# Optimization experiments

Hardware: AMD Instinct MI355X
Metric: run time of the kernel (lower is better)

The kernel has to match this reference:

```python
import jax, jax.numpy as jnp
import numpy as np

N_NODES = 50000
N_EDGES = 800000
IN_CH, HID_CH, OUT_CH = 128, 256, 128


def setup_inputs() -> dict:
    key = jax.random.key(0)
    ks = jax.random.split(key, 9)
    x = jax.random.normal(ks[0], (N_NODES, IN_CH), dtype=jnp.float32)
    edge_index = jax.random.randint(ks[1], (2, N_EDGES), 0, N_NODES, dtype=jnp.int64)
    # SAGEConv params: lin_l (aggregated neighbors, with bias), lin_r (root, no bias)
    s1 = 1.0 / np.sqrt(IN_CH)
    s2 = 1.0 / np.sqrt(HID_CH)
    W1_l = jax.random.uniform(ks[2], (IN_CH, HID_CH), jnp.float32, -s1, s1)
    W1_r = jax.random.uniform(ks[3], (IN_CH, HID_CH), jnp.float32, -s1, s1)
    b1 = jax.random.uniform(ks[4], (HID_CH,), jnp.float32, -s1, s1)
    W2_l = jax.random.uniform(ks[5], (HID_CH, OUT_CH), jnp.float32, -s2, s2)
    W2_r = jax.random.uniform(ks[6], (HID_CH, OUT_CH), jnp.float32, -s2, s2)
    b2 = jax.random.uniform(ks[7], (OUT_CH,), jnp.float32, -s2, s2)
    return {"x": x, "edge_index": edge_index, "W1_l": W1_l, "W1_r": W1_r,
            "b1": b1, "W2_l": W2_l, "W2_r": W2_r, "b2": b2}


def _sage_conv(x, edge_index, Wl, Wr, b):
    # PyG SAGEConv: out = lin_l(mean_{j in N(i)} x_j) + lin_r(x_i)
    src, dst = edge_index[0], edge_index[1]
    msg = x[src]                                                    # [E, C] gather
    agg = jax.ops.segment_sum(msg, dst, num_segments=x.shape[0])    # [N, C] scatter-add
    cnt = jax.ops.segment_sum(jnp.ones((src.shape[0],), x.dtype), dst,
                              num_segments=x.shape[0])              # [N]
    agg = agg / jnp.maximum(cnt, 1.0)[:, None]                      # mean; deg-0 -> 0
    return agg @ Wl + x @ Wr + b


def reference(x, edge_index, W1_l, W1_r, b1, W2_l, W2_r, b2):
    h = jax.nn.relu(_sage_conv(x, edge_index, W1_l, W1_r, b1))
    # dropout(p=0.5) is stochastic; use eval-mode identity for a deterministic baseline
    out = _sage_conv(h, edge_index, W2_l, W2_r, b2)
    return jax.nn.log_softmax(out, axis=1)
```

## Files before the change

### kernel.cpp

```cpp
#include <hip/hip_runtime.h>
#include <math.h>

#define NN 50000
#define NE 800000
#define BINW 256
#define NB ((NN + BINW - 1) / BINW)
#define CAP 4864
#define CHUNK 4096
#define NBIN ((NE + CHUNK - 1) / CHUNK)
#define NXB 6250
#define NWB 256
#define EPT 16

typedef __attribute__((ext_vector_type(8))) _Float16 f16x8;
typedef __attribute__((ext_vector_type(2))) _Float16 h2;
typedef __attribute__((ext_vector_type(4))) float f32x4;
typedef unsigned int uint32;
typedef __attribute__((address_space(3))) unsigned int lds_uint;
typedef const __attribute__((address_space(1))) unsigned int glb_uint;

__device__ inline unsigned short f2h(float f) {
    _Float16 h = (_Float16)f;
    return __builtin_bit_cast(unsigned short, h);
}
__device__ inline uint32 pack2h(float a, float b) {
    return (uint32)f2h(a) | ((uint32)f2h(b) << 16);
}
__device__ inline h2 as_h2(uint32 u) { return __builtin_bit_cast(h2, u); }

__device__ inline int edge_at(const void* edges, int is64, int i) {
    return is64 ? (int)((const long long*)edges)[i] : ((const int*)edges)[i];
}

__global__ void k_zero(int* bcnt) {
    int i = threadIdx.x;
    if (i < NB) bcnt[i] = 0;
}

__global__ __launch_bounds__(256)
void k_front(const void* __restrict__ edges, uint32* __restrict__ gbuf,
             int* __restrict__ bcnt,
             const float* __restrict__ x, unsigned short* __restrict__ A1,
             const float* __restrict__ W1l, const float* __restrict__ W1r,
             const float* __restrict__ W2l, const float* __restrict__ W2r,
             unsigned short* __restrict__ B1t, unsigned short* __restrict__ B2t) {
    int b = blockIdx.x;
    if (b >= NBIN) {
        if (b < NBIN + NXB) {
            int t = (b - NBIN) * 256 + threadIdx.x;
            if (t >= NN * 32) return;
            int node = t >> 5, q = t & 31;
            float4 v = *(const float4*)(x + (size_t)node * 128 + q * 4);
            *(uint2*)(A1 + (size_t)node * 256 + 128 + q * 4) =
                make_uint2(pack2h(v.x, v.y), pack2h(v.z, v.w));
        } else {
            int t = (b - NBIN - NXB) * 256 + threadIdx.x;
            int n = t >> 8, k = t & 255;
            float v1 = (k < 128) ? W1l[k * 256 + n] : W1r[(k - 128) * 256 + n];
            B1t[n * 256 + k] = f2h(v1);
            float v2 = (n < 128) ? W2l[k * 128 + n] : W2r[k * 128 + (n - 128)];
            B2t[n * 256 + k] = f2h(v2);
        }
        return;
    }
    __shared__ int hist[NB], excl[NB], cur[NB], gpos[NB];
    __shared__ int is64s;
    __shared__ uint32 sorted[CHUNK];
    int t = threadIdx.x;
    int base = b * CHUNK;
    int n = NE - base; if (n > CHUNK) n = CHUNK;
    if (t < 64) {
        const long long* q = (const long long*)edges;
        long long v = q[t];
        unsigned long long m = __ballot(v >= 0 && v < NN);
        if (t == 0) is64s = (m == ~0ull) ? 1 : 0;
    }
    for (int i = t; i < NB; i += 256) hist[i] = 0;
    __syncthreads();
    int is64 = is64s;
    int sA[EPT], dA[EPT];
    #pragma unroll
    for (int q = 0; q < EPT; ++q) {
        int i = t + q * 256;
        if (i < n) {
            sA[q] = edge_at(edges, is64, base + i);
            dA[q] = edge_at(edges, is64, NE + base + i);
        } else dA[q] = -1;
    }
    #pragma unroll
    for (int q = 0; q < EPT; ++q)
        if (dA[q] >= 0) atomicAdd(&hist[dA[q] >> 8], 1);
    __syncthreads();
    if (t == 0) {
        int s = 0;
        for (int k = 0; k < NB; ++k) { excl[k] = s; s += hist[k]; }
    }
    __syncthreads();
    for (int i = t; i < NB; i += 256) {
        gpos[i] = atomicAdd(&bcnt[i], hist[i]);
        cur[i] = excl[i];
    }
    __syncthreads();
    #pragma unroll
    for (int q = 0; q < EPT; ++q) {
        if (dA[q] >= 0) {
            int bk = dA[q] >> 8;
            int lp = atomicAdd(&cur[bk], 1);
            sorted[lp] = ((uint32)(dA[q] & (BINW - 1)) << 16) | (uint32)sA[q];
        }
    }
    __syncthreads();
    for (int i = t; i < n; i += 256) {
        int lo = 0, hi = NB - 1;
        while (lo < hi) { int mid = (lo + hi + 1) >> 1; if (excl[mid] <= i) lo = mid; else hi = mid - 1; }
        int gp = gpos[lo] + (i - excl[lo]);
        if (gp < CAP) gbuf[(size_t)lo * CAP + gp] = sorted[i];
    }
}

__global__ __launch_bounds__(256) void k_sort(const uint32* __restrict__ gbuf,
                                              const int* __restrict__ bcnt,
                                              int* __restrict__ offs,
                                              unsigned short* __restrict__ ssrc) {
    __shared__ int hist[BINW], cur[BINW], wsum[4];
    __shared__ int sorted[CAP];
    __shared__ int bb_s;
    int b = blockIdx.x, t = threadIdx.x;
    int lane = t & 63, w = t >> 6;
    int c = (t < NB) ? bcnt[t] : 0;
    int pre = (t < b) ? c : 0;
    #pragma unroll
    for (int s = 1; s < 64; s <<= 1) pre += __shfl_xor(pre, s);
    if (lane == 0) wsum[w] = pre;
    hist[t] = 0;
    __syncthreads();
    if (t == 0) bb_s = wsum[0] + wsum[1] + wsum[2] + wsum[3];
    __syncthreads();
    int bb = bb_s;
    int cnt = bcnt[b]; if (cnt > CAP) cnt = CAP;
    int nbase = b * BINW;
    int ncnt = NN - nbase; if (ncnt > BINW) ncnt = BINW;
    for (int i = t; i < cnt; i += 256)
        atomicAdd(&hist[gbuf[(size_t)b * CAP + i] >> 16], 1);
    __syncthreads();
    int d = hist[t];
    int v = d;
    #pragma unroll
    for (int s = 1; s < 64; s <<= 1) { int x = __shfl_up(v, s); if (lane >= s) v += x; }
    if (lane == 63) wsum[w] = v;
    __syncthreads();
    if (t == 0) { int s = 0; for (int i = 0; i < 4; ++i) { int x = wsum[i]; wsum[i] = s; s += x; } }
    __syncthreads();
    int excl = wsum[w] + (v - d);
    if (t < ncnt) offs[nbase + t] = bb + excl;
    if (b == NB - 1 && t == 0) offs[NN] = NE;
    cur[t] = excl;
    __syncthreads();
    for (int i = t; i < cnt; i += 256) {
        uint32 p = gbuf[(size_t)b * CAP + i];
        int lp = atomicAdd(&cur[p >> 16], 1);
        sorted[lp] = (int)(p & 0xFFFFu);
    }
    __syncthreads();
    for (int i = t; i < cnt; i += 256)
        ssrc[bb + i] = (unsigned short)sorted[i];
}

#define ACCH(vv) { a[0] += as_h2((vv).x); a[1] += as_h2((vv).y); \
                   a[2] += as_h2((vv).z); a[3] += as_h2((vv).w); }

__device__ inline void burst_gather4(const unsigned short* __restrict__ tab, int coff,
                                     const unsigned short* __restrict__ ssrc, int s0, int s1,
                                     int lane, h2* a) {
    int grp = lane >> 4, cl = lane & 15;
    const unsigned short* bp = tab + coff + cl * 8;
    int e = s0;
    while (e < s1) {
        int cnt = s1 - e; if (cnt > 64) cnt = 64;
        int myidx = (lane < cnt) ? (int)ssrc[e + lane] : 0;
        for (int r0 = 0; r0 < cnt; r0 += 32) {
            uint4 v[8]; bool ok[8];
            #pragma unroll
            for (int u = 0; u < 8; ++u) {
                int r = r0 + u * 4 + grp;
                ok[u] = r < cnt;
                int s = __shfl(myidx, r & 63);
                v[u] = *(const uint4*)(bp + (size_t)s * 256);
            }
            #pragma unroll
            for (int u = 0; u < 8; ++u) if (ok[u]) ACCH(v[u]);
        }
        e += cnt;
    }
}

__device__ inline void xreduce_h(h2* a) {
    #pragma unroll
    for (int k = 0; k < 4; ++k) {
        uint32 u = __builtin_bit_cast(uint32, a[k]);
        a[k] += as_h2((uint32)__shfl_xor((int)u, 16));
        u = __builtin_bit_cast(uint32, a[k]);
        a[k] += as_h2((uint32)__shfl_xor((int)u, 32));
    }
}

__global__ void k_agg(unsigned short* __restrict__ A1, const int* __restrict__ offs,
                      const unsigned short* __restrict__ ssrc) {
    int node = blockIdx.x * 4 + (threadIdx.x >> 6);
    int lane = threadIdx.x & 63;
    if (node >= NN) return;
    int cl = lane & 15;
    int s0 = offs[node], s1 = offs[node + 1];
    h2 a[4] = {};
    burst_gather4(A1, 128, ssrc, s0, s1, lane, a);
    xreduce_h(a);
    float inv = 1.0f / fmaxf((float)(s1 - s0), 1.0f);
    if (lane < 16) {
        uint4 p;
        p.x = pack2h((float)a[0][0] * inv, (float)a[0][1] * inv);
        p.y = pack2h((float)a[1][0] * inv, (float)a[1][1] * inv);
        p.z = pack2h((float)a[2][0] * inv, (float)a[2][1] * inv);
        p.w = pack2h((float)a[3][0] * inv, (float)a[3][1] * inv);
        *(uint4*)(A1 + (size_t)node * 256 + cl * 8) = p;
    }
}

template <bool RELU>
__global__ __launch_bounds__(256)
void k_gemm_bf(const unsigned short* __restrict__ A, const unsigned short* __restrict__ Bt,
               const float* __restrict__ bias, unsigned short* __restrict__ C) {
    __shared__ unsigned short AsmL[3][128 * 32];
    __shared__ unsigned short BsmL[3][128 * 32];
    int t = threadIdx.x;
    int lane = t & 63, w = t >> 6;
    int m0 = blockIdx.x * 128, n0 = blockIdx.y * 128;
    int wr = (w >> 1) * 64, wc = (w & 1) * 64;
    int fr = lane & 15, fk = (lane >> 4) * 8;

    f32x4 acc[4][4] = {};
    int srow = lane >> 2;
    int scol = (lane & 3) * 8;
    auto STAGE = [&](int bufi, int ks) {
        #pragma unroll
        for (int q = 0; q < 2; ++q) {
            int widx = w * 2 + q;
            int row = widx * 16 + srow;
            const unsigned short* ga = A + (size_t)(m0 + row) * 256 + ks * 32 + scol;
            __builtin_amdgcn_global_load_lds((glb_uint*)ga, (lds_uint*)&AsmL[bufi][widx * 512], 16, 0, 0);
            const unsigned short* gb = Bt + (size_t)(n0 + row) * 256 + ks * 32 + scol;
            __builtin_amdgcn_global_load_lds((glb_uint*)gb, (lds_uint*)&BsmL[bufi][widx * 512], 16, 0, 0);
        }
    };

    STAGE(0, 0);
    STAGE(1, 1);
    #pragma unroll
    for (int ks = 0; ks < 8; ++ks) {
        if (ks < 7) asm volatile("s_waitcnt vmcnt(4)" ::: "memory");
        else        asm volatile("s_waitcnt vmcnt(0)" ::: "memory");
        __builtin_amdgcn_s_barrier();
        __builtin_amdgcn_sched_barrier(0);
        if (ks < 6) STAGE((ks + 2) % 3, ks + 2);
        int cb = ks % 3;
        f16x8 af[4], bfr[4];
        #pragma unroll
        for (int i = 0; i < 4; ++i) af[i] = *(const f16x8*)&AsmL[cb][(wr + i * 16 + fr) * 32 + fk];
        #pragma unroll
        for (int j = 0; j < 4; ++j) bfr[j] = *(const f16x8*)&BsmL[cb][(wc + j * 16 + fr) * 32 + fk];
        #pragma unroll
        for (int i = 0; i < 4; ++i)
            #pragma unroll
            for (int j = 0; j < 4; ++j)
                acc[i][j] = __builtin_amdgcn_mfma_f32_16x16x32_f16(af[i], bfr[j], acc[i][j], 0, 0, 0);
    }

    int r0 = (lane >> 4) * 4;
    #pragma unroll
    for (int i = 0; i < 4; ++i) {
        #pragma unroll
        for (int j = 0; j < 4; ++j) {
            int gn = n0 + wc + j * 16 + fr;
            float bb = RELU ? bias[gn] : 0.f;
            #pragma unroll
            for (int rr = 0; rr < 4; ++rr) {
                int gm = m0 + wr + i * 16 + r0 + rr;
                if (gm >= NN) continue;
                float v = acc[i][j][rr];
                if (RELU) v = fmaxf(v + bb, 0.f);
                C[(size_t)gm * 256 + gn] = f2h(v);
            }
        }
    }
}

__global__ void k_final(const unsigned short* __restrict__ P, const int* __restrict__ offs,
                        const unsigned short* __restrict__ ssrc, const float* __restrict__ b2,
                        float* __restrict__ out) {
    int node = blockIdx.x * 4 + (threadIdx.x >> 6);
    int lane = threadIdx.x & 63;
    if (node >= NN) return;
    int cl = lane & 15;
    int s0 = offs[node], s1 = offs[node + 1];
    h2 a[4] = {};
    burst_gather4(P, 0, ssrc, s0, s1, lane, a);
    xreduce_h(a);
    float inv = 1.0f / fmaxf((float)(s1 - s0), 1.0f);
    uint4 rv = *(const uint4*)(P + (size_t)node * 256 + 128 + cl * 8);
    float4 ba = *(const float4*)(b2 + cl * 8);
    float4 bb = *(const float4*)(b2 + cl * 8 + 4);
    h2 r0 = as_h2(rv.x), r1 = as_h2(rv.y), r2 = as_h2(rv.z), r3 = as_h2(rv.w);
    float vv[8];
    vv[0] = (float)a[0][0] * inv + (float)r0[0] + ba.x;
    vv[1] = (float)a[0][1] * inv + (float)r0[1] + ba.y;
    vv[2] = (float)a[1][0] * inv + (float)r1[0] + ba.z;
    vv[3] = (float)a[1][1] * inv + (float)r1[1] + ba.w;
    vv[4] = (float)a[2][0] * inv + (float)r2[0] + bb.x;
    vv[5] = (float)a[2][1] * inv + (float)r2[1] + bb.y;
    vv[6] = (float)a[3][0] * inv + (float)r3[0] + bb.z;
    vv[7] = (float)a[3][1] * inv + (float)r3[1] + bb.w;

    float mx = vv[0];
    #pragma unroll
    for (int k = 1; k < 8; ++k) mx = fmaxf(mx, vv[k]);
    #pragma unroll
    for (int d = 1; d < 16; d <<= 1) mx = fmaxf(mx, __shfl_xor(mx, d));
    float s = 0.f;
    #pragma unroll
    for (int k = 0; k < 8; ++k) s += __expf(vv[k] - mx);
    #pragma unroll
    for (int d = 1; d < 16; d <<= 1) s += __shfl_xor(s, d);
    float ls = logf(s);
    if (lane < 16) {
        float4 o0 = make_float4(vv[0] - mx - ls, vv[1] - mx - ls, vv[2] - mx - ls, vv[3] - mx - ls);
        float4 o1 = make_float4(vv[4] - mx - ls, vv[5] - mx - ls, vv[6] - mx - ls, vv[7] - mx - ls);
        *(float4*)(out + (size_t)node * 128 + cl * 8) = o0;
        *(float4*)(out + (size_t)node * 128 + cl * 8 + 4) = o1;
    }
}

extern "C" void kernel_launch(void* const* d_in, const int* in_sizes, int n_in,
                              void* d_out, int out_size, void* d_ws, size_t ws_size,
                              hipStream_t stream) {
    const float* x   = (const float*)d_in[0];
    const void*  edg = d_in[1];
    const float* W1l = (const float*)d_in[2];
    const float* W1r = (const float*)d_in[3];
    const float* b1  = (const float*)d_in[4];
    const float* W2l = (const float*)d_in[5];
    const float* W2r = (const float*)d_in[6];
    const float* b2  = (const float*)d_in[7];
    float* out = (float*)d_out;

    char* ws = (char*)d_ws;
    size_t off = 0;
    auto alloc = [&](size_t bytes) {
        size_t cur = off;
        off = (off + bytes + 255) & ~(size_t)255;
        return cur;
    };
    int* bcnt  = (int*)(ws + alloc((size_t)NB * 4));
    int* offs  = (int*)(ws + alloc((size_t)(NN + 1) * 4));
    unsigned short* ssrc = (unsigned short*)(ws + alloc((size_t)NE * 2));
    uint32* gbuf = (uint32*)(ws + alloc((size_t)NB * CAP * 4));
    unsigned short* A1  = (unsigned short*)(ws + alloc((size_t)NN * 256 * 2));
    unsigned short* Hb  = (unsigned short*)(ws + alloc((size_t)NN * 256 * 2));
    unsigned short* Pb  = (unsigned short*)(ws + alloc((size_t)NN * 256 * 2));
    unsigned short* B1t = (unsigned short*)(ws + alloc((size_t)65536 * 2));
    unsigned short* B2t = (unsigned short*)(ws + alloc((size_t)65536 * 2));
    (void)alloc(65536);

    int nb_w = (NN + 3) / 4;
    int mblocks = (NN + 127) / 128;

    k_zero<<<1, 256, 0, stream>>>(bcnt);
    k_front<<<NBIN + NXB + NWB, 256, 0, stream>>>(edg, gbuf, bcnt, x, A1,
                                                  W1l, W1r, W2l, W2r, B1t, B2t);
    k_sort<<<NB, 256, 0, stream>>>(gbuf, bcnt, offs, ssrc);
    k_agg<<<nb_w, 256, 0, stream>>>(A1, offs, ssrc);
    k_gemm_bf<true><<<dim3(mblocks, 2), 256, 0, stream>>>(A1, B1t, b1, Hb);
    k_gemm_bf<false><<<dim3(mblocks, 2), 256, 0, stream>>>(Hb, B2t, nullptr, Pb);
    k_final<<<nb_w, 256, 0, stream>>>(Pb, offs, ssrc, b2, out);
}
```

Measured before the change: 147.7 us.

## Map four nodes per wavefront in aggregation and final gather kernels

Each 64-lane wavefront now handles four nodes, with one 16-lane group per node, instead of one node per wavefront with a cross-group shuffle reduction. Neighbor indices are staged in registers and broadcast with shuffles, and degrees above 32 fall back to direct index loads. This removes the xor-shuffle reduction and the idle lanes during stores, and cuts the grid to a quarter of its size. In exchange, the loop runs to the maximum degree among the four nodes, which adds divergence, and the launch relies on NN being divisible by 16 with no bounds check.

```diff
diff --git a/kernel.cpp b/kernel.cpp
--- a/kernel.cpp
+++ b/kernel.cpp
@@ -166,63 +166,60 @@
         ssrc[bb + i] = (unsigned short)sorted[i];
 }
 
-#define ACCH(vv) { a[0] += as_h2((vv).x); a[1] += as_h2((vv).y); \
-                   a[2] += as_h2((vv).z); a[3] += as_h2((vv).w); }
-
-__device__ inline void burst_gather4(const unsigned short* __restrict__ tab, int coff,
-                                     const unsigned short* __restrict__ ssrc, int s0, int s1,
-                                     int lane, h2* a) {
-    int grp = lane >> 4, cl = lane & 15;
-    const unsigned short* bp = tab + coff + cl * 8;
-    int e = s0;
-    while (e < s1) {
-        int cnt = s1 - e; if (cnt > 64) cnt = 64;
-        int myidx = (lane < cnt) ? (int)ssrc[e + lane] : 0;
-        for (int r0 = 0; r0 < cnt; r0 += 32) {
-            uint4 v[8]; bool ok[8];
-            #pragma unroll
-            for (int u = 0; u < 8; ++u) {
-                int r = r0 + u * 4 + grp;
-                ok[u] = r < cnt;
-                int s = __shfl(myidx, r & 63);
-                v[u] = *(const uint4*)(bp + (size_t)s * 256);
-            }
-            #pragma unroll
-            for (int u = 0; u < 8; ++u) if (ok[u]) ACCH(v[u]);
-        }
-        e += cnt;
-    }
-}
-
-__device__ inline void xreduce_h(h2* a) {
-    #pragma unroll
-    for (int k = 0; k < 4; ++k) {
-        uint32 u = __builtin_bit_cast(uint32, a[k]);
-        a[k] += as_h2((uint32)__shfl_xor((int)u, 16));
-        u = __builtin_bit_cast(uint32, a[k]);
-        a[k] += as_h2((uint32)__shfl_xor((int)u, 32));
+#define ACCH1(vv) { a[0] += as_h2((vv).x); a[1] += as_h2((vv).y); \
+                    a[2] += as_h2((vv).z); a[3] += as_h2((vv).w); }
+
+__device__ inline void group_gather(const unsigned short* __restrict__ tab, int coff,
+                                    const unsigned short* __restrict__ ssrc,
+                                    int s0, int deg, int md, int grp, int lig, h2* a) {
+    const unsigned short* bp = tab + coff + lig * 8;
+    int idxA = (lig < deg)      ? (int)ssrc[s0 + lig]      : 0;
+    int idxB = (16 + lig < deg) ? (int)ssrc[s0 + 16 + lig] : 0;
+    int cap = md < 32 ? md : 32;
+    for (int i0 = 0; i0 < cap; i0 += 8) {
+        uint4 v[8];
+        #pragma unroll
+        for (int u = 0; u < 8; ++u) {
+            int i = i0 + u;
+            int word = (i & 16) ? idxB : idxA;
+            int s = __shfl(word, grp * 16 + (i & 15));
+            v[u] = *(const uint4*)(bp + (size_t)s * 256);
+        }
+        #pragma unroll
+        for (int u = 0; u < 8; ++u) if (i0 + u < deg) ACCH1(v[u]);
+    }
+    for (int i0 = 32; i0 < md; i0 += 4) {
+        uint4 v[4];
+        #pragma unroll
+        for (int u = 0; u < 4; ++u) {
+            int i = i0 + u;
+            int s = (i < deg) ? (int)ssrc[s0 + i] : 0;
+            v[u] = *(const uint4*)(bp + (size_t)s * 256);
+        }
+        #pragma unroll
+        for (int u = 0; u < 4; ++u) if (i0 + u < deg) ACCH1(v[u]);
     }
 }
 
 __global__ void k_agg(unsigned short* __restrict__ A1, const int* __restrict__ offs,
                       const unsigned short* __restrict__ ssrc) {
-    int node = blockIdx.x * 4 + (threadIdx.x >> 6);
     int lane = threadIdx.x & 63;
-    if (node >= NN) return;
-    int cl = lane & 15;
-    int s0 = offs[node], s1 = offs[node + 1];
+    int grp = lane >> 4, lig = lane & 15;
+    int wid = (blockIdx.x * 256 + threadIdx.x) >> 6;
+    int node = wid * 4 + grp;
+    int s0 = offs[node], deg = offs[node + 1] - s0;
+    int md = deg;
+    md = max(md, __shfl_xor(md, 16));
+    md = max(md, __shfl_xor(md, 32));
     h2 a[4] = {};
-    burst_gather4(A1, 128, ssrc, s0, s1, lane, a);
-    xreduce_h(a);
-    float inv = 1.0f / fmaxf((float)(s1 - s0), 1.0f);
-    if (lane < 16) {
-        uint4 p;
-        p.x = pack2h((float)a[0][0] * inv, (float)a[0][1] * inv);
-        p.y = pack2h((float)a[1][0] * inv, (float)a[1][1] * inv);
-        p.z = pack2h((float)a[2][0] * inv, (float)a[2][1] * inv);
-        p.w = pack2h((float)a[3][0] * inv, (float)a[3][1] * inv);
-        *(uint4*)(A1 + (size_t)node * 256 + cl * 8) = p;
-    }
+    group_gather(A1, 128, ssrc, s0, deg, md, grp, lig, a);
+    float inv = 1.0f / fmaxf((float)deg, 1.0f);
+    uint4 p;
+    p.x = pack2h((float)a[0][0] * inv, (float)a[0][1] * inv);
+    p.y = pack2h((float)a[1][0] * inv, (float)a[1][1] * inv);
+    p.z = pack2h((float)a[2][0] * inv, (float)a[2][1] * inv);
+    p.w = pack2h((float)a[3][0] * inv, (float)a[3][1] * inv);
+    *(uint4*)(A1 + (size_t)node * 256 + lig * 8) = p;
 }
 
 template <bool RELU>
@@ -296,18 +293,20 @@
 __global__ void k_final(const unsigned short* __restrict__ P, const int* __restrict__ offs,
                         const unsigned short* __restrict__ ssrc, const float* __restrict__ b2,
                         float* __restrict__ out) {
-    int node = blockIdx.x * 4 + (threadIdx.x >> 6);
     int lane = threadIdx.x & 63;
-    if (node >= NN) return;
-    int cl = lane & 15;
-    int s0 = offs[node], s1 = offs[node + 1];
+    int grp = lane >> 4, lig = lane & 15;
+    int wid = (blockIdx.x * 256 + threadIdx.x) >> 6;
+    int node = wid * 4 + grp;
+    int s0 = offs[node], deg = offs[node + 1] - s0;
+    int md = deg;
+    md = max(md, __shfl_xor(md, 16));
+    md = max(md, __shfl_xor(md, 32));
     h2 a[4] = {};
-    burst_gather4(P, 0, ssrc, s0, s1, lane, a);
-    xreduce_h(a);
-    float inv = 1.0f / fmaxf((float)(s1 - s0), 1.0f);
-    uint4 rv = *(const uint4*)(P + (size_t)node * 256 + 128 + cl * 8);
-    float4 ba = *(const float4*)(b2 + cl * 8);
-    float4 bb = *(const float4*)(b2 + cl * 8 + 4);
+    group_gather(P, 0, ssrc, s0, deg, md, grp, lig, a);
+    float inv = 1.0f / fmaxf((float)deg, 1.0f);
+    uint4 rv = *(const uint4*)(P + (size_t)node * 256 + 128 + lig * 8);
+    float4 ba = *(const float4*)(b2 + lig * 8);
+    float4 bb = *(const float4*)(b2 + lig * 8 + 4);
     h2 r0 = as_h2(rv.x), r1 = as_h2(rv.y), r2 = as_h2(rv.z), r3 = as_h2(rv.w);
     float vv[8];
     vv[0] = (float)a[0][0] * inv + (float)r0[0] + ba.x;
@@ -330,12 +329,10 @@
     #pragma unroll
     for (int d = 1; d < 16; d <<= 1) s += __shfl_xor(s, d);
     float ls = logf(s);
-    if (lane < 16) {
-        float4 o0 = make_float4(vv[0] - mx - ls, vv[1] - mx - ls, vv[2] - mx - ls, vv[3] - mx - ls);
-        float4 o1 = make_float4(vv[4] - mx - ls, vv[5] - mx - ls, vv[6] - mx - ls, vv[7] - mx - ls);
-        *(float4*)(out + (size_t)node * 128 + cl * 8) = o0;
-        *(float4*)(out + (size_t)node * 128 + cl * 8 + 4) = o1;
-    }
+    float4 o0 = make_float4(vv[0] - mx - ls, vv[1] - mx - ls, vv[2] - mx - ls, vv[3] - mx - ls);
+    float4 o1 = make_float4(vv[4] - mx - ls, vv[5] - mx - ls, vv[6] - mx - ls, vv[7] - mx - ls);
+    *(float4*)(out + (size_t)node * 128 + lig * 8) = o0;
+    *(float4*)(out + (size_t)node * 128 + lig * 8 + 4) = o1;
 }
 
 extern "C" void kernel_launch(void* const* d_in, const int* in_sizes, int n_in,
@@ -369,15 +366,15 @@
     unsigned short* B2t = (unsigned short*)(ws + alloc((size_t)65536 * 2));
     (void)alloc(65536);
 
-    int nb_w = (NN + 3) / 4;
+    int nb_g = NN / 16;
     int mblocks = (NN + 127) / 128;
 
     k_zero<<<1, 256, 0, stream>>>(bcnt);
     k_front<<<NBIN + NXB + NWB, 256, 0, stream>>>(edg, gbuf, bcnt, x, A1,
                                                   W1l, W1r, W2l, W2r, B1t, B2t);
     k_sort<<<NB, 256, 0, stream>>>(gbuf, bcnt, offs, ssrc);
-    k_agg<<<nb_w, 256, 0, stream>>>(A1, offs, ssrc);
+    k_agg<<<nb_g, 256, 0, stream>>>(A1, offs, ssrc);
     k_gemm_bf<true><<<dim3(mblocks, 2), 256, 0, stream>>>(A1, B1t, b1, Hb);
     k_gemm_bf<false><<<dim3(mblocks, 2), 256, 0, stream>>>(Hb, B2t, nullptr, Pb);
-    k_final<<<nb_w, 256, 0, stream>>>(Pb, offs, ssrc, b2, out);
-}
+    k_final<<<nb_g, 256, 0, stream>>>(Pb, offs, ssrc, b2, out);
+}
```

After: 146.0 us. No clear change (-1.2%).
